# Kernel tuning notes

Hardware: AMD Instinct MI355X
Metric: run time of the kernel (lower is better)

Reference implementation:

```python
import jax, jax.numpy as jnp
import numpy as np

EMBED = 1024
HEADS = 16
HEAD_DIM = EMBED // HEADS


def setup_inputs() -> dict:
    key = jax.random.key(0)
    ks = jax.random.split(key, 6)
    B, T, C = 4, 2048, EMBED
    x = jax.random.normal(ks[0], (B, T, C), dtype=jnp.float32)
    # random binary mask [B,1,1,T]; keep at least one valid key per row by forcing first position to 1
    mask = jax.random.randint(ks[1], (B, 1, 1, T), 0, 2, dtype=jnp.int32)
    mask = mask.at[..., 0].set(1)
    scale = 1.0 / np.sqrt(C)
    qkv_w = jax.random.normal(ks[2], (3 * C, C), dtype=jnp.float32) * scale  # torch Linear weight [out,in]
    qkv_b = jax.random.normal(ks[3], (3 * C,), dtype=jnp.float32) * scale
    out_w = jax.random.normal(ks[4], (C, C), dtype=jnp.float32) * scale
    out_b = jax.random.normal(ks[5], (C,), dtype=jnp.float32) * scale
    return {"x": x, "mask": mask, "qkv_w": qkv_w, "qkv_b": qkv_b, "out_w": out_w, "out_b": out_b}


def reference(x, mask, qkv_w, qkv_b, out_w, out_b):
    B, T, C = x.shape
    H, D = HEADS, HEAD_DIM
    qkv = x @ qkv_w.T + qkv_b  # [B,T,3C]
    qkv = qkv.reshape(B, T, 3, H, D).transpose(2, 0, 3, 1, 4)  # [3,B,H,T,D]
    q, k, v = qkv[0], qkv[1], qkv[2]
    scores = jnp.einsum('bhqd,bhkd->bhqk', q, k) / np.sqrt(D)
    scores = jnp.where(mask == 0, -jnp.inf, scores)
    attn = jax.nn.softmax(scores, axis=-1)
    out = jnp.einsum('bhqk,bhkd->bhqd', attn, v)
    out = out.transpose(0, 2, 1, 3).reshape(B, T, C)
    return out @ out_w.T + out_b
```

## Files before the change

kernel.cpp:

```cpp
#include <hip/hip_runtime.h>
#include <hip/hip_bf16.h>

typedef _Float16 f16;
typedef _Float16 f16x4_t __attribute__((ext_vector_type(4)));
typedef _Float16 f16x8 __attribute__((ext_vector_type(8)));
typedef float f32x4 __attribute__((ext_vector_type(4)));

#define AS1(p) ((const __attribute__((address_space(1))) void*)(p))
#define AS3(p) ((__attribute__((address_space(3))) void*)(p))

__device__ __forceinline__ void gload_lds16(const f16* g, f16* l) {
    __builtin_amdgcn_global_load_lds(AS1(g), AS3(l), 16, 0, 0);
}

__device__ __forceinline__ f16x8 cvt8(float4 u, float4 v) {
    f16x8 r;
    r[0] = (f16)u.x; r[1] = (f16)u.y; r[2] = (f16)u.z; r[3] = (f16)u.w;
    r[4] = (f16)v.x; r[5] = (f16)v.y; r[6] = (f16)v.z; r[7] = (f16)v.w;
    return r;
}

#define Q_SCALE 0.180336880111f

__global__ __launch_bounds__(64) void scan_mask(
    const int* __restrict__ mask, int* __restrict__ cpos, int* __restrict__ nkv)
{
    const int b = blockIdx.x;
    const int lane = threadIdx.x;
    const int* mb = mask + b * 2048;
    int run = 0;
    for (int c = 0; c < 2048; c += 64) {
        int v = (mb[c + lane] != 0) ? 1 : 0;
        unsigned long long bits = __ballot(v);
        int pre = __popcll(bits & ((1ull << lane) - 1ull));
        cpos[b * 2048 + c + lane] = v ? (run + pre) : -1;
        run += __popcll(bits);
    }
    if (lane == 0) nkv[b] = run;
}

__global__ __launch_bounds__(256) void fill_tail(
    const int* __restrict__ nkv, f16* __restrict__ k_c, f16* __restrict__ vt_c)
{
    const int b = blockIdx.x, h = blockIdx.y;
    const int run = nkv[b];
    const int pad = (run + 63) & ~63;
    const int tail = pad - run;
    if (tail == 0) return;
    const int tid = threadIdx.x;
    const size_t bh = (size_t)(b * 16 + h);
    f16x8 z = {};
    f16* kp = k_c + bh * (size_t)(2048 * 64) + (size_t)run * 64;
    const int kn = tail * 64;
    for (int x = tid * 8; x < kn; x += 256 * 8)
        *(f16x8*)&kp[x] = z;
    const int wave = tid >> 6, lane = tid & 63;
    for (int d = wave; d < 64; d += 4) {
        f16* vp = vt_c + (bh * 64 + d) * 2048 + run;
        if (lane < tail) vp[lane] = (f16)0.f;
    }
}

__global__ __launch_bounds__(256) void gemm_qkv_f16(
    const float* __restrict__ A, const float* __restrict__ Bw,
    const float* __restrict__ bias, const int* __restrict__ cpos,
    f16* __restrict__ q_g, f16* __restrict__ k_g, f16* __restrict__ vt_g,
    int M, int K)
{
    constexpr int BK = 32, LDK = 40;
    __shared__ f16 As[128 * LDK], Bs[128 * LDK];

    const int tid  = threadIdx.x;
    const int lane = tid & 63, wave = tid >> 6;
    const int wy = wave >> 1, wx = wave & 1;
    const int lrow = lane & 15, quad = lane >> 4;
    const int lin = (int)(blockIdx.y * 24 + blockIdx.x);
    const int swz = (lin & 7) * 192 + (lin >> 3);
    const size_t m0 = (size_t)(swz / 24) * 128;
    const size_t n0 = (size_t)(swz % 24) * 128;
    const int r0 = tid >> 2;
    const int kc = (tid & 3) * 8;
    const size_t s64K = (size_t)64 * K;

    const float* pa = &A [(m0 + r0) * K + kc];
    const float* pb = &Bw[(n0 + r0) * K + kc];
    float4 a00 = *(const float4*)pa;
    float4 a01 = *(const float4*)(pa + 4);
    float4 a10 = *(const float4*)(pa + s64K);
    float4 a11 = *(const float4*)(pa + s64K + 4);
    float4 b00 = *(const float4*)pb;
    float4 b01 = *(const float4*)(pb + 4);
    float4 b10 = *(const float4*)(pb + s64K);
    float4 b11 = *(const float4*)(pb + s64K + 4);

    f32x4 acc[4][4] = {};

    for (int k0 = 0; k0 < K; k0 += BK) {
        __syncthreads();
        *(f16x8*)&As[ r0       * LDK + kc] = cvt8(a00, a01);
        *(f16x8*)&As[(r0 + 64) * LDK + kc] = cvt8(a10, a11);
        *(f16x8*)&Bs[ r0       * LDK + kc] = cvt8(b00, b01);
        *(f16x8*)&Bs[(r0 + 64) * LDK + kc] = cvt8(b10, b11);
        __syncthreads();

        if (k0 + BK < K) {
            pa += BK; pb += BK;
            a00 = *(const float4*)pa;
            a01 = *(const float4*)(pa + 4);
            a10 = *(const float4*)(pa + s64K);
            a11 = *(const float4*)(pa + s64K + 4);
            b00 = *(const float4*)pb;
            b01 = *(const float4*)(pb + 4);
            b10 = *(const float4*)(pb + s64K);
            b11 = *(const float4*)(pb + s64K + 4);
        }

        f16x8 af[4], bf[4];
#pragma unroll
        for (int i = 0; i < 4; ++i)
            af[i] = *(const f16x8*)&As[(wy * 64 + i * 16 + lrow) * LDK + quad * 8];
#pragma unroll
        for (int j = 0; j < 4; ++j)
            bf[j] = *(const f16x8*)&Bs[(wx * 64 + j * 16 + lrow) * LDK + quad * 8];
#pragma unroll
        for (int i = 0; i < 4; ++i)
#pragma unroll
            for (int j = 0; j < 4; ++j)
                acc[i][j] = __builtin_amdgcn_mfma_f32_16x16x32_f16(af[i], bf[j], acc[i][j], 0, 0, 0);
    }

    const int region = (int)(n0 >> 10);
#pragma unroll
    for (int i = 0; i < 4; ++i) {
        size_t row = m0 + wy * 64 + i * 16 + quad * 4;
        int b = (int)(row >> 11);
        int t = (int)(row & 2047);
        int cp[4];
        if (region != 0) {
            int4 c4 = *(const int4*)&cpos[b * 2048 + t];
            cp[0] = c4.x; cp[1] = c4.y; cp[2] = c4.z; cp[3] = c4.w;
        }
#pragma unroll
        for (int j = 0; j < 4; ++j) {
            int col = (int)n0 + wx * 64 + j * 16 + lrow;
            float bb = bias[col];
            int cl = col & 1023, hh = cl >> 6, d = cl & 63;
            if (region == 0) {
                size_t o = ((size_t)(b * 16 + hh) * 2048 + t) * 64 + d;
#pragma unroll
                for (int r = 0; r < 4; ++r)
                    q_g[o + (size_t)r * 64] = (f16)((acc[i][j][r] + bb) * Q_SCALE);
            } else if (region == 1) {
#pragma unroll
                for (int r = 0; r < 4; ++r)
                    if (cp[r] >= 0)
                        k_g[((size_t)(b * 16 + hh) * 2048 + cp[r]) * 64 + d] =
                            (f16)(acc[i][j][r] + bb);
            } else {
#pragma unroll
                for (int r = 0; r < 4; ++r)
                    if (cp[r] >= 0)
                        vt_g[((size_t)(b * 16 + hh) * 64 + d) * 2048 + cp[r]] =
                            (f16)(acc[i][j][r] + bb);
            }
        }
    }
}

__global__ __launch_bounds__(256) void gemm2_f16(
    const f16* __restrict__ A, const float* __restrict__ Bw,
    const float* __restrict__ bias, float* __restrict__ C,
    int M, int N, int K)
{
    constexpr int BK = 32, LDK = 40;
    __shared__ f16 As[128 * LDK], Bs[128 * LDK];

    const int tid  = threadIdx.x;
    const int lane = tid & 63, wave = tid >> 6;
    const int wy = wave >> 1, wx = wave & 1;
    const int lrow = lane & 15, quad = lane >> 4;
    const int lin = (int)(blockIdx.y * 8 + blockIdx.x);
    const int swz = (lin & 7) * 64 + (lin >> 3);
    const size_t m0 = (size_t)(swz >> 3) * 128;
    const size_t n0 = (size_t)(swz & 7) * 128;
    const int r0 = tid >> 2;
    const int kc = (tid & 3) * 8;
    const size_t s64K = (size_t)64 * K;

    const f16*   pa = &A [(m0 + r0) * K + kc];
    const float* pb = &Bw[(n0 + r0) * K + kc];
    f16x8 ga0 = *(const f16x8*)pa;
    f16x8 ga1 = *(const f16x8*)(pa + s64K);
    float4 b00 = *(const float4*)pb;
    float4 b01 = *(const float4*)(pb + 4);
    float4 b10 = *(const float4*)(pb + s64K);
    float4 b11 = *(const float4*)(pb + s64K + 4);

    f32x4 acc[4][4] = {};

    for (int k0 = 0; k0 < K; k0 += BK) {
        __syncthreads();
        *(f16x8*)&As[ r0       * LDK + kc] = ga0;
        *(f16x8*)&As[(r0 + 64) * LDK + kc] = ga1;
        *(f16x8*)&Bs[ r0       * LDK + kc] = cvt8(b00, b01);
        *(f16x8*)&Bs[(r0 + 64) * LDK + kc] = cvt8(b10, b11);
        __syncthreads();

        if (k0 + BK < K) {
            pa += BK; pb += BK;
            ga0 = *(const f16x8*)pa;
            ga1 = *(const f16x8*)(pa + s64K);
            b00 = *(const float4*)pb;
            b01 = *(const float4*)(pb + 4);
            b10 = *(const float4*)(pb + s64K);
            b11 = *(const float4*)(pb + s64K + 4);
        }

        f16x8 af[4], bf[4];
#pragma unroll
        for (int i = 0; i < 4; ++i)
            af[i] = *(const f16x8*)&As[(wy * 64 + i * 16 + lrow) * LDK + quad * 8];
#pragma unroll
        for (int j = 0; j < 4; ++j)
            bf[j] = *(const f16x8*)&Bs[(wx * 64 + j * 16 + lrow) * LDK + quad * 8];
#pragma unroll
        for (int i = 0; i < 4; ++i)
#pragma unroll
            for (int j = 0; j < 4; ++j)
                acc[i][j] = __builtin_amdgcn_mfma_f32_16x16x32_f16(af[i], bf[j], acc[i][j], 0, 0, 0);
    }

#pragma unroll
    for (int i = 0; i < 4; ++i) {
        size_t row = m0 + wy * 64 + i * 16 + quad * 4;
#pragma unroll
        for (int j = 0; j < 4; ++j) {
            size_t col = n0 + wx * 64 + j * 16 + lrow;
            float bb = bias[col];
#pragma unroll
            for (int r = 0; r < 4; ++r)
                C[(row + r) * N + col] = acc[i][j][r] + bb;
        }
    }
}

__global__ __launch_bounds__(256) void attn_f16(
    const f16* __restrict__ q_g, const f16* __restrict__ k_g,
    const f16* __restrict__ vt_g, const int* __restrict__ nkv,
    f16* __restrict__ att, int B, int T)
{
    constexpr int LDP = 72;
    __shared__ f16 Ks_s[2][64 * 64];
    __shared__ f16 Vt_s[2][64 * 64];
    __shared__ f16 Pt[128 * LDP];

    const int tid  = threadIdx.x;
    const int lane = tid & 63, wave = tid >> 6;
    const int lrow = lane & 15, quad = lane >> 4;
    const int bid = ((int)blockIdx.x & 7) * 128 + ((int)blockIdx.x >> 3);
    const int qt = bid & 15;
    const int h  = (bid >> 4) & 15;
    const int b  = bid >> 8;
    const size_t base = (size_t)b * T;
    const size_t bh = (size_t)(b * 16 + h);
    const f16* qg_base = q_g  + bh * (2048 * 64);
    const f16* kg_base = k_g  + bh * (2048 * 64);
    const f16* vt_base = vt_g + bh * (64 * 2048);

    const int nk = nkv[b];
    const int ntiles = (nk + 63) >> 6;

    const int x0 = ((quad)     ^ (lrow & 7)) * 8;
    const int x1 = ((4 + quad) ^ (lrow & 7)) * 8;

    f16x8 aq[2][2];
#pragma unroll
    for (int qi = 0; qi < 2; ++qi)
#pragma unroll
        for (int ks = 0; ks < 2; ++ks)
            aq[qi][ks] = *(const f16x8*)&qg_base[
                (size_t)(qt * 128 + wave * 32 + qi * 16 + lrow) * 64 + ks * 32 + quad * 8];

    f32x4 oacc[2][4] = {};
    float l_part[2] = {0.f, 0.f};

    const int srow0 = (lane >> 3);
    const int sgrp  = (lane & 7);

    auto stage = [&](int kt, int bsel) {
        const f16* kT = kg_base + kt * 4096;
#pragma unroll
        for (int j = 0; j < 2; ++j) {
            int rg  = wave + j * 4;
            int row = rg * 8 + srow0;
            int grp = sgrp ^ (row & 7);
            gload_lds16(&kT[row * 64 + grp * 8], &Ks_s[bsel][rg * 512 + lane * 8]);
            gload_lds16(&vt_base[(size_t)row * 2048 + kt * 64 + grp * 8],
                        &Vt_s[bsel][rg * 512 + lane * 8]);
        }
    };

    stage(0, 0);
    __syncthreads();

    for (int kt = 0; kt < ntiles; ++kt) {
        const int cur = kt & 1;
        if (kt + 1 < ntiles) stage(kt + 1, cur ^ 1);

        const f16* Ks = Ks_s[cur];
        const f16* Vt = Vt_s[cur];

        f32x4 s[2][4];
        __builtin_amdgcn_s_setprio(1);
#pragma unroll
        for (int ni = 0; ni < 4; ++ni) {
            const int key = ni * 16 + lrow;
            f16x8 k0 = *(const f16x8*)&Ks[key * 64 + x0];
            f16x8 k1 = *(const f16x8*)&Ks[key * 64 + x1];
#pragma unroll
            for (int qi = 0; qi < 2; ++qi) {
                f32x4 t = {0.f, 0.f, 0.f, 0.f};
                t = __builtin_amdgcn_mfma_f32_16x16x32_f16(k0, aq[qi][0], t, 0, 0, 0);
                t = __builtin_amdgcn_mfma_f32_16x16x32_f16(k1, aq[qi][1], t, 0, 0, 0);
                s[qi][ni] = t;
            }
        }
        __builtin_amdgcn_s_setprio(0);

        const int rem = nk - kt * 64;
        auto softmax = [&](bool masked) {
#pragma unroll
            for (int qi = 0; qi < 2; ++qi)
#pragma unroll
                for (int ni = 0; ni < 4; ++ni) {
                    float p[4];
#pragma unroll
                    for (int r = 0; r < 4; ++r) {
                        float e = __builtin_amdgcn_exp2f(s[qi][ni][r]);
                        p[r] = (!masked || (ni * 16 + quad * 4 + r) < rem) ? e : 0.f;
                    }
                    l_part[qi] += (p[0] + p[1]) + (p[2] + p[3]);
                    f16x4_t pk;
#pragma unroll
                    for (int r = 0; r < 4; ++r) pk[r] = (f16)p[r];
                    *(f16x4_t*)&Pt[(wave * 32 + qi * 16 + lrow) * LDP + ni * 16 + quad * 4] = pk;
                }
        };
        if (rem >= 64) softmax(false); else softmax(true);

        f16x8 pf[2][2];
#pragma unroll
        for (int qi = 0; qi < 2; ++qi)
#pragma unroll
            for (int ks = 0; ks < 2; ++ks)
                pf[qi][ks] = *(const f16x8*)&Pt[(wave * 32 + qi * 16 + lrow) * LDP + ks * 32 + quad * 8];
        __builtin_amdgcn_s_setprio(1);
#pragma unroll
        for (int di = 0; di < 4; ++di) {
            const int d = di * 16 + lrow;
            f16x8 v0 = *(const f16x8*)&Vt[d * 64 + x0];
            f16x8 v1 = *(const f16x8*)&Vt[d * 64 + x1];
#pragma unroll
            for (int qi = 0; qi < 2; ++qi) {
                oacc[qi][di] = __builtin_amdgcn_mfma_f32_16x16x32_f16(v0, pf[qi][0], oacc[qi][di], 0, 0, 0);
                oacc[qi][di] = __builtin_amdgcn_mfma_f32_16x16x32_f16(v1, pf[qi][1], oacc[qi][di], 0, 0, 0);
            }
        }
        __builtin_amdgcn_s_setprio(0);

        __syncthreads();
    }

#pragma unroll
    for (int qi = 0; qi < 2; ++qi) {
        float v = l_part[qi];
        v += __shfl_xor(v, 16);
        v += __shfl_xor(v, 32);
        float inv = 1.f / v;
        int q = qt * 128 + wave * 32 + qi * 16 + lrow;
#pragma unroll
        for (int di = 0; di < 4; ++di) {
            f16x4_t o;
#pragma unroll
            for (int r = 0; r < 4; ++r) o[r] = (f16)(oacc[qi][di][r] * inv);
            *(f16x4_t*)&att[(base + q) * 1024 + h * 64 + di * 16 + quad * 4] = o;
        }
    }
}

extern "C" void kernel_launch(void* const* d_in, const int* in_sizes, int n_in,
                              void* d_out, int out_size, void* d_ws, size_t ws_size,
                              hipStream_t stream) {
    const float* x     = (const float*)d_in[0];
    const int*   mask  = (const int*)d_in[1];
    const float* qkv_w = (const float*)d_in[2];
    const float* qkv_b = (const float*)d_in[3];
    const float* out_w = (const float*)d_in[4];
    const float* out_b = (const float*)d_in[5];
    float* out = (float*)d_out;

    const int B = 4, T = 2048;
    const int M = B * T;
    char* ws = (char*)d_ws;
    f16* q_g = (f16*)(ws);
    f16* k_g = (f16*)(ws + 16777216);
    f16* vt  = (f16*)(ws + 33554432);
    f16* att = (f16*)(ws + 50331648);

    int* cpos = (int*)d_out;
    int* nkv  = cpos + 4 * 2048;

    dim3 blk(256);
    scan_mask<<<dim3(4), dim3(64), 0, stream>>>(mask, cpos, nkv);
    fill_tail<<<dim3(4, 16), blk, 0, stream>>>(nkv, k_g, vt);
    gemm_qkv_f16<<<dim3(3072 / 128, M / 128), blk, 0, stream>>>(x, qkv_w, qkv_b, cpos, q_g, k_g, vt, M, 1024);
    attn_f16<<<dim3(B * 16 * 16), blk, 0, stream>>>(q_g, k_g, vt, nkv, att, B, T);
    gemm2_f16<<<dim3(1024 / 128, M / 128), blk, 0, stream>>>(att, out_w, out_b, out, M, 1024, 1024);
}
```

Measured before the change: 295.6 us.

## Pre-convert GEMM operands to f16 and load tiles via direct global-to-LDS

Adds a conversion kernel that turns x, qkv_w and out_w into f16 copies up front, written to scratch space in the output buffer and in the q buffer, which is free again once attention has run. Both GEMMs then load 64-wide K tiles straight into XOR-swizzled shared memory with global_load_lds, replacing the register-staged fp32 loads with in-loop conversion. BK doubles and the block-index swizzle is dropped. This trades extra conversion passes and extra global traffic for a leaner GEMM inner loop, but the new loads are issued right before a barrier, so global-load prefetch overlap with compute is lost.

```diff
diff --git a/kernel.cpp b/kernel.cpp
--- a/kernel.cpp
+++ b/kernel.cpp
@@ -21,6 +21,19 @@
 }
 
 #define Q_SCALE 0.180336880111f
+
+__global__ __launch_bounds__(256) void cvt_f32_f16(
+    const float* __restrict__ src, f16* __restrict__ dst, int n8)
+{
+    int idx = blockIdx.x * 256 + threadIdx.x;
+    int stride = gridDim.x * 256;
+    for (int i = idx; i < n8; i += stride) {
+        size_t o = (size_t)i * 8;
+        float4 u = *(const float4*)&src[o];
+        float4 v = *(const float4*)&src[o + 4];
+        *(f16x8*)&dst[o] = cvt8(u, v);
+    }
+}
 
 __global__ __launch_bounds__(64) void scan_mask(
     const int* __restrict__ mask, int* __restrict__ cpos, int* __restrict__ nkv)
@@ -62,71 +75,61 @@
 }
 
 __global__ __launch_bounds__(256) void gemm_qkv_f16(
-    const float* __restrict__ A, const float* __restrict__ Bw,
+    const f16* __restrict__ A16, const f16* __restrict__ Bw16,
     const float* __restrict__ bias, const int* __restrict__ cpos,
     f16* __restrict__ q_g, f16* __restrict__ k_g, f16* __restrict__ vt_g,
     int M, int K)
 {
-    constexpr int BK = 32, LDK = 40;
-    __shared__ f16 As[128 * LDK], Bs[128 * LDK];
+    constexpr int BK = 64;
+    __shared__ f16 As[128 * BK], Bs[128 * BK];
 
     const int tid  = threadIdx.x;
     const int lane = tid & 63, wave = tid >> 6;
     const int wy = wave >> 1, wx = wave & 1;
     const int lrow = lane & 15, quad = lane >> 4;
-    const int lin = (int)(blockIdx.y * 24 + blockIdx.x);
-    const int swz = (lin & 7) * 192 + (lin >> 3);
-    const size_t m0 = (size_t)(swz / 24) * 128;
-    const size_t n0 = (size_t)(swz % 24) * 128;
-    const int r0 = tid >> 2;
-    const int kc = (tid & 3) * 8;
-    const size_t s64K = (size_t)64 * K;
-
-    const float* pa = &A [(m0 + r0) * K + kc];
-    const float* pb = &Bw[(n0 + r0) * K + kc];
-    float4 a00 = *(const float4*)pa;
-    float4 a01 = *(const float4*)(pa + 4);
-    float4 a10 = *(const float4*)(pa + s64K);
-    float4 a11 = *(const float4*)(pa + s64K + 4);
-    float4 b00 = *(const float4*)pb;
-    float4 b01 = *(const float4*)(pb + 4);
-    float4 b10 = *(const float4*)(pb + s64K);
-    float4 b11 = *(const float4*)(pb + s64K + 4);
+    const size_t m0 = (size_t)blockIdx.y * 128;
+    const size_t n0 = (size_t)blockIdx.x * 128;
+    const int srow = lane >> 3;
+    const int sgrp = lane & 7;
+    const int x0 = ((quad)     ^ (lrow & 7)) * 8;
+    const int x1 = ((4 + quad) ^ (lrow & 7)) * 8;
 
     f32x4 acc[4][4] = {};
 
     for (int k0 = 0; k0 < K; k0 += BK) {
         __syncthreads();
-        *(f16x8*)&As[ r0       * LDK + kc] = cvt8(a00, a01);
-        *(f16x8*)&As[(r0 + 64) * LDK + kc] = cvt8(a10, a11);
-        *(f16x8*)&Bs[ r0       * LDK + kc] = cvt8(b00, b01);
-        *(f16x8*)&Bs[(r0 + 64) * LDK + kc] = cvt8(b10, b11);
+#pragma unroll
+        for (int j = 0; j < 4; ++j) {
+            int rg  = wave * 4 + j;
+            int row = rg * 8 + srow;
+            int grp = sgrp ^ srow;
+            gload_lds16(&A16[(m0 + row) * (size_t)K + k0 + grp * 8],
+                        &As[rg * 512 + lane * 8]);
+            gload_lds16(&Bw16[(n0 + row) * (size_t)K + k0 + grp * 8],
+                        &Bs[rg * 512 + lane * 8]);
+        }
         __syncthreads();
 
-        if (k0 + BK < K) {
-            pa += BK; pb += BK;
-            a00 = *(const float4*)pa;
-            a01 = *(const float4*)(pa + 4);
-            a10 = *(const float4*)(pa + s64K);
-            a11 = *(const float4*)(pa + s64K + 4);
-            b00 = *(const float4*)pb;
-            b01 = *(const float4*)(pb + 4);
-            b10 = *(const float4*)(pb + s64K);
-            b11 = *(const float4*)(pb + s64K + 4);
-        }
-
-        f16x8 af[4], bf[4];
+        f16x8 a0[4], a1[4], b0[4], b1[4];
+#pragma unroll
+        for (int i = 0; i < 4; ++i) {
+            const int r = (wy * 64 + i * 16 + lrow) * BK;
+            a0[i] = *(const f16x8*)&As[r + x0];
+            a1[i] = *(const f16x8*)&As[r + x1];
+        }
+#pragma unroll
+        for (int j = 0; j < 4; ++j) {
+            const int r = (wx * 64 + j * 16 + lrow) * BK;
+            b0[j] = *(const f16x8*)&Bs[r + x0];
+            b1[j] = *(const f16x8*)&Bs[r + x1];
+        }
 #pragma unroll
         for (int i = 0; i < 4; ++i)
-            af[i] = *(const f16x8*)&As[(wy * 64 + i * 16 + lrow) * LDK + quad * 8];
-#pragma unroll
-        for (int j = 0; j < 4; ++j)
-            bf[j] = *(const f16x8*)&Bs[(wx * 64 + j * 16 + lrow) * LDK + quad * 8];
-#pragma unroll
-        for (int i = 0; i < 4; ++i)
-#pragma unroll
-            for (int j = 0; j < 4; ++j)
-                acc[i][j] = __builtin_amdgcn_mfma_f32_16x16x32_f16(af[i], bf[j], acc[i][j], 0, 0, 0);
+#pragma unroll
+            for (int j = 0; j < 4; ++j) {
+                acc[i][j] = __builtin_amdgcn_mfma_f32_16x16x32_f16(a0[i], b0[j], acc[i][j], 0, 0, 0);
+                acc[i][j] = __builtin_amdgcn_mfma_f32_16x16x32_f16(a1[i], b1[j], acc[i][j], 0, 0, 0);
+            }
     }
 
     const int region = (int)(n0 >> 10);
@@ -168,66 +171,59 @@
 }
 
 __global__ __launch_bounds__(256) void gemm2_f16(
-    const f16* __restrict__ A, const float* __restrict__ Bw,
+    const f16* __restrict__ A16, const f16* __restrict__ Bw16,
     const float* __restrict__ bias, float* __restrict__ C,
     int M, int N, int K)
 {
-    constexpr int BK = 32, LDK = 40;
-    __shared__ f16 As[128 * LDK], Bs[128 * LDK];
+    constexpr int BK = 64;
+    __shared__ f16 As[128 * BK], Bs[128 * BK];
 
     const int tid  = threadIdx.x;
     const int lane = tid & 63, wave = tid >> 6;
     const int wy = wave >> 1, wx = wave & 1;
     const int lrow = lane & 15, quad = lane >> 4;
-    const int lin = (int)(blockIdx.y * 8 + blockIdx.x);
-    const int swz = (lin & 7) * 64 + (lin >> 3);
-    const size_t m0 = (size_t)(swz >> 3) * 128;
-    const size_t n0 = (size_t)(swz & 7) * 128;
-    const int r0 = tid >> 2;
-    const int kc = (tid & 3) * 8;
-    const size_t s64K = (size_t)64 * K;
-
-    const f16*   pa = &A [(m0 + r0) * K + kc];
-    const float* pb = &Bw[(n0 + r0) * K + kc];
-    f16x8 ga0 = *(const f16x8*)pa;
-    f16x8 ga1 = *(const f16x8*)(pa + s64K);
-    float4 b00 = *(const float4*)pb;
-    float4 b01 = *(const float4*)(pb + 4);
-    float4 b10 = *(const float4*)(pb + s64K);
-    float4 b11 = *(const float4*)(pb + s64K + 4);
+    const size_t m0 = (size_t)blockIdx.y * 128;
+    const size_t n0 = (size_t)blockIdx.x * 128;
+    const int srow = lane >> 3, sgrp = lane & 7;
+    const int x0 = ((quad)     ^ (lrow & 7)) * 8;
+    const int x1 = ((4 + quad) ^ (lrow & 7)) * 8;
 
     f32x4 acc[4][4] = {};
 
     for (int k0 = 0; k0 < K; k0 += BK) {
         __syncthreads();
-        *(f16x8*)&As[ r0       * LDK + kc] = ga0;
-        *(f16x8*)&As[(r0 + 64) * LDK + kc] = ga1;
-        *(f16x8*)&Bs[ r0       * LDK + kc] = cvt8(b00, b01);
-        *(f16x8*)&Bs[(r0 + 64) * LDK + kc] = cvt8(b10, b11);
+#pragma unroll
+        for (int j = 0; j < 4; ++j) {
+            int rg  = wave * 4 + j;
+            int row = rg * 8 + srow;
+            int grp = sgrp ^ srow;
+            gload_lds16(&A16[(m0 + row) * (size_t)K + k0 + grp * 8],
+                        &As[rg * 512 + lane * 8]);
+            gload_lds16(&Bw16[(n0 + row) * (size_t)K + k0 + grp * 8],
+                        &Bs[rg * 512 + lane * 8]);
+        }
         __syncthreads();
 
-        if (k0 + BK < K) {
-            pa += BK; pb += BK;
-            ga0 = *(const f16x8*)pa;
-            ga1 = *(const f16x8*)(pa + s64K);
-            b00 = *(const float4*)pb;
-            b01 = *(const float4*)(pb + 4);
-            b10 = *(const float4*)(pb + s64K);
-            b11 = *(const float4*)(pb + s64K + 4);
-        }
-
-        f16x8 af[4], bf[4];
+        f16x8 a0[4], a1[4], b0[4], b1[4];
+#pragma unroll
+        for (int i = 0; i < 4; ++i) {
+            const int r = (wy * 64 + i * 16 + lrow) * BK;
+            a0[i] = *(const f16x8*)&As[r + x0];
+            a1[i] = *(const f16x8*)&As[r + x1];
+        }
+#pragma unroll
+        for (int j = 0; j < 4; ++j) {
+            const int r = (wx * 64 + j * 16 + lrow) * BK;
+            b0[j] = *(const f16x8*)&Bs[r + x0];
+            b1[j] = *(const f16x8*)&Bs[r + x1];
+        }
 #pragma unroll
         for (int i = 0; i < 4; ++i)
-            af[i] = *(const f16x8*)&As[(wy * 64 + i * 16 + lrow) * LDK + quad * 8];
-#pragma unroll
-        for (int j = 0; j < 4; ++j)
-            bf[j] = *(const f16x8*)&Bs[(wx * 64 + j * 16 + lrow) * LDK + quad * 8];
-#pragma unroll
-        for (int i = 0; i < 4; ++i)
-#pragma unroll
-            for (int j = 0; j < 4; ++j)
-                acc[i][j] = __builtin_amdgcn_mfma_f32_16x16x32_f16(af[i], bf[j], acc[i][j], 0, 0, 0);
+#pragma unroll
+            for (int j = 0; j < 4; ++j) {
+                acc[i][j] = __builtin_amdgcn_mfma_f32_16x16x32_f16(a0[i], b0[j], acc[i][j], 0, 0, 0);
+                acc[i][j] = __builtin_amdgcn_mfma_f32_16x16x32_f16(a1[i], b1[j], acc[i][j], 0, 0, 0);
+            }
     }
 
 #pragma unroll
@@ -407,13 +403,19 @@
     f16* vt  = (f16*)(ws + 33554432);
     f16* att = (f16*)(ws + 50331648);
 
-    int* cpos = (int*)d_out;
+    f16* x16 = (f16*)d_out;
+    f16* w16 = (f16*)((char*)d_out + 16777216);
+    int* cpos = (int*)((char*)d_out + 23068672);
     int* nkv  = cpos + 4 * 2048;
+    f16* ow16 = q_g;
 
     dim3 blk(256);
+    cvt_f32_f16<<<dim3(2048), blk, 0, stream>>>(x, x16, M * 1024 / 8);
+    cvt_f32_f16<<<dim3(1024), blk, 0, stream>>>(qkv_w, w16, 3072 * 1024 / 8);
     scan_mask<<<dim3(4), dim3(64), 0, stream>>>(mask, cpos, nkv);
     fill_tail<<<dim3(4, 16), blk, 0, stream>>>(nkv, k_g, vt);
-    gemm_qkv_f16<<<dim3(3072 / 128, M / 128), blk, 0, stream>>>(x, qkv_w, qkv_b, cpos, q_g, k_g, vt, M, 1024);
+    gemm_qkv_f16<<<dim3(3072 / 128, M / 128), blk, 0, stream>>>(x16, w16, qkv_b, cpos, q_g, k_g, vt, M, 1024);
     attn_f16<<<dim3(B * 16 * 16), blk, 0, stream>>>(q_g, k_g, vt, nkv, att, B, T);
-    gemm2_f16<<<dim3(1024 / 128, M / 128), blk, 0, stream>>>(att, out_w, out_b, out, M, 1024, 1024);
-}
+    cvt_f32_f16<<<dim3(512), blk, 0, stream>>>(out_w, ow16, 1024 * 1024 / 8);
+    gemm2_f16<<<dim3(1024 / 128, M / 128), blk, 0, stream>>>(att, ow16, out_b, out, M, 1024, 1024);
+}
```

Measured after the change: 279.5 us. 1.06x faster.
